# Performance work log

Hardware: AMD Instinct MI355X
Metric: run time of the kernel (lower is better)

The kernel has to match this reference:

```python
import jax, jax.numpy as jnp
import numpy as np

GH, GW = 1024, 1024  # image-like grid graph, N = GH*GW nodes


def _grid_edge_index(h, w):
    idx = np.arange(h * w, dtype=np.int32).reshape(h, w)
    r = np.concatenate([idx[:, :-1].ravel(), idx[:, 1:].ravel(), idx[:-1, :].ravel(), idx[1:, :].ravel()])
    c = np.concatenate([idx[:, 1:].ravel(), idx[:, :-1].ravel(), idx[1:, :].ravel(), idx[:-1, :].ravel()])
    return np.stack([r, c]).astype(np.int32)


def setup_inputs():
    key = jax.random.key(0)
    ks = jax.random.split(key, 10)
    n = GH * GW
    ei = jnp.asarray(_grid_edge_index(GH, GW))
    yy, xx = np.meshgrid(np.arange(GH), np.arange(GW), indexing="ij")
    pos = jnp.asarray((np.stack([xx, yy], -1).reshape(n, 2) / float(GH)).astype(np.float32))
    x = jax.random.normal(ks[0], (n, 5), jnp.float32)
    s1, s2, s3, s4 = 5 ** -0.5, 16 ** -0.5, 32 ** -0.5, 8 ** -0.5
    return {
        "x": x, "pos": pos, "edge_index": ei,
        "W1": jax.random.normal(ks[1], (5, 16), jnp.float32) * s1,
        "W1r": jax.random.normal(ks[2], (5, 16), jnp.float32) * s1,
        "b1": jnp.zeros((16,), jnp.float32),
        "W2": jax.random.normal(ks[3], (16, 32), jnp.float32) * s2,
        "W2r": jax.random.normal(ks[4], (16, 32), jnp.float32) * s2,
        "b2": jnp.zeros((32,), jnp.float32),
        "lin1_w": jax.random.normal(ks[5], (32, 8), jnp.float32) * s3,
        "lin1_b": jnp.zeros((8,), jnp.float32),
        "lin2_w": jax.random.normal(ks[6], (8, 2), jnp.float32) * s4,
        "lin2_b": jnp.zeros((2,), jnp.float32),
    }


def _spline_conv_k1(x, row, col, evalid, W, Wr, b, n):
    # SplineConv(dim=1, kernel_size=1): single basis fn == 1, edge_attr cancels.
    # out_i = mean_{(j->i)} x_j @ W + x_i @ Wr + b   (aggr='mean', target = col)
    xw = x @ W
    seg = jnp.where(evalid, col, n)  # invalid edges -> dump segment n
    msg = jnp.where(evalid[:, None], xw[row], 0.0)
    s = jax.ops.segment_sum(msg, seg, num_segments=n + 1)[:n]
    cnt = jax.ops.segment_sum(evalid.astype(x.dtype), seg, num_segments=n + 1)[:n]
    return s / jnp.maximum(cnt, 1.0)[:, None] + x @ Wr + b


def _normalized_cut(row, col, edge_attr, evalid, n):
    seg = jnp.where(evalid, row, n)
    deg = jax.ops.segment_sum(evalid.astype(edge_attr.dtype), seg, num_segments=n + 1)[:n]
    inv = jnp.where(deg > 0, 1.0 / jnp.maximum(deg, 1.0), 0.0)
    return edge_attr * (inv[row] + inv[col])


def _heavy_edge_match(row, col, w, evalid, n):
    # graclus-style heavy-edge matching, deterministic parallel mutual-max variant:
    # each node proposes its max-weight neighbor; mutual proposals merge.
    ar = jnp.arange(n, dtype=jnp.int32)
    seg = jnp.where(evalid, row, n)
    wm = jnp.where(evalid, w, -jnp.inf)
    best = jax.ops.segment_max(wm, seg, num_segments=n + 1)[:n]
    is_best = evalid & (w == best[row])
    partner = jax.ops.segment_min(jnp.where(is_best, col, n), seg, num_segments=n + 1)[:n]
    partner = jnp.where(partner >= n, ar, partner).astype(jnp.int32)
    mutual = partner[partner] == ar
    return jnp.where(mutual, jnp.minimum(ar, partner), ar)


def _forward(x, pos, edge_index, W1, W1r, b1, W2, W2r, b2, lin1_w, lin1_b, lin2_w, lin2_b):
    n = x.shape[0]
    row, col = edge_index[0], edge_index[1]
    ev0 = jnp.ones(row.shape[0], dtype=bool)
    ar = jnp.arange(n, dtype=jnp.int32)

    # GNN1: relu(SplineConv) then LeakyReLU(0.1)
    x1 = jax.nn.leaky_relu(jax.nn.relu(_spline_conv_k1(x, row, col, ev0, W1, W1r, b1, n)), 0.1)

    # normalized_cut_2d on 1-d pseudo-pos x0[:,0]; graclus; max_pool
    attr1 = jnp.abs(x[row, 0] - x[col, 0])
    c1 = _heavy_edge_match(row, col, _normalized_cut(row, col, attr1, ev0, n), ev0, n)
    valid1 = c1 == ar
    xp = jax.ops.segment_max(x1, c1, num_segments=n)  # cluster-wise max pool
    xp = jnp.where(valid1[:, None], xp, 0.0)
    cnt1 = jax.ops.segment_sum(jnp.ones((n,), x.dtype), c1, num_segments=n)
    posp = jax.ops.segment_sum(pos, c1, num_segments=n) / jnp.maximum(cnt1, 1.0)[:, None]
    row2, col2 = c1[row], c1[col]
    ev2 = row2 != col2  # drop intra-cluster (self-loop) edges

    # GNN2 (kernel_size=1 => pooled Cartesian edge_attr unused) + LeakyReLU(0.1)
    x2 = jax.nn.leaky_relu(jax.nn.relu(_spline_conv_k1(xp, row2, col2, ev2, W2, W2r, b2, n)), 0.1)

    # normalized_cut on pooled 2-d pos; graclus; max_pool_x; global_mean_pool
    d = posp[row2] - posp[col2]
    attr2 = jnp.sqrt(jnp.sum(d * d, axis=1) + 1e-12)
    c2 = _heavy_edge_match(row2, col2, _normalized_cut(row2, col2, attr2, ev2, n), ev2, n)
    seg2 = jnp.where(valid1, c2, n)
    x3 = jax.ops.segment_max(x2, seg2, num_segments=n + 1)[:n]
    cnt2 = jax.ops.segment_sum(valid1.astype(x.dtype), seg2, num_segments=n + 1)[:n]
    valid2 = cnt2 > 0
    x3 = jnp.where(valid2[:, None], x3, 0.0)
    pooled = jnp.sum(x3, axis=0) / jnp.sum(valid2.astype(x.dtype))  # single graph -> mean over clusters

    h = jax.nn.leaky_relu(pooled @ lin1_w + lin1_b, 0.1)
    return h @ lin2_w + lin2_b  # == x[0], shape [2]


def reference(x, pos, edge_index, W1, W1r, b1, W2, W2r, b2, lin1_w, lin1_b, lin2_w, lin2_b):
    return _forward(x, pos, edge_index, W1, W1r, b1, W2, W2r, b2, lin1_w, lin1_b, lin2_w, lin2_b)
```

## Files before the change

### kernel.cpp

```cpp
#include <hip/hip_runtime.h>
#include <math.h>

typedef long long i64;
typedef unsigned long long u64;

#define GWD 1024
#define GMSK 1023
#define GSH 10

__device__ __forceinline__ int xcd_band(int b, int nb) {
  return (b & 7) * (nb >> 3) + (b >> 3);
}

__device__ __forceinline__ int deg_of(int m) {
  int xx = m & GMSK, yy = m >> GSH;
  return (xx > 0) + (xx < GMSK) + (yy > 0) + (yy < GMSK);
}

__global__ __launch_bounds__(256)
void kA_match1(const float* __restrict__ x, int* __restrict__ partner1, int n) {
#pragma clang fp contract(off)
  int m = xcd_band(blockIdx.x, gridDim.x) * 256 + threadIdx.x;
  if (m >= n) return;
  int xx = m & GMSK, yy = m >> GSH;
  bool vW = xx > 0, vE = xx < GMSK, vN = yy > 0, vS = yy < GMSK;
  int cnt = (int)vW + (int)vE + (int)vN + (int)vS;
  float invi = 1.0f / (float)cnt;
  float xm0 = x[(i64)m * 5];
  float best = -INFINITY;
  int pr = n;
#define NB1(valid, J)                                                  \
  if (valid) {                                                         \
    int j = (J);                                                       \
    float a0 = x[(i64)j * 5];                                          \
    float w = fabsf(xm0 - a0) * (invi + 1.0f / (float)deg_of(j));      \
    if (w > best) { best = w; pr = j; }                                \
  }
  NB1(vN, m - GWD)
  NB1(vW, m - 1)
  NB1(vE, m + 1)
  NB1(vS, m + GWD)
#undef NB1
  partner1[m] = pr;
}

__device__ __forceinline__ void conv1_static(const float* __restrict__ x, int m,
                                             const float* w1, const float* w1r,
                                             const float* b1, float (&out)[16]) {
  int xx = m & GMSK, yy = m >> GSH;
  bool vW = xx > 0, vE = xx < GMSK, vN = yy > 0, vS = yy < GMSK;
  int cnt = (int)vW + (int)vE + (int)vN + (int)vS;
  float s0 = 0.f, s1 = 0.f, s2 = 0.f, s3 = 0.f, s4 = 0.f;
#define ACC1(valid, J)                                     \
  if (valid) {                                             \
    const float* xj = x + (i64)(J) * 5;                    \
    s0 += xj[0]; s1 += xj[1]; s2 += xj[2];                 \
    s3 += xj[3]; s4 += xj[4];                              \
  }
  ACC1(vN, m - GWD)
  ACC1(vW, m - 1)
  ACC1(vE, m + 1)
  ACC1(vS, m + GWD)
#undef ACC1
  const float* xm = x + (i64)m * 5;
  float m0 = xm[0], m1 = xm[1], m2 = xm[2], m3 = xm[3], m4 = xm[4];
  float cf = (float)cnt;
#pragma unroll
  for (int f = 0; f < 16; ++f) {
    float a  = s0 * w1[f] + s1 * w1[16 + f] + s2 * w1[32 + f] + s3 * w1[48 + f] + s4 * w1[64 + f];
    float rt = m0 * w1r[f] + m1 * w1r[16 + f] + m2 * w1r[32 + f] + m3 * w1r[48 + f] + m4 * w1r[64 + f];
    out[f] = fmaxf(a / cf + rt + b1[f], 0.0f);
  }
}

__global__ __launch_bounds__(256)
void kB_pool1(const float* __restrict__ x, const float* __restrict__ pos,
              const int* __restrict__ partner1,
              const float* __restrict__ W1, const float* __restrict__ W1r,
              const float* __restrict__ b1,
              int* __restrict__ c1, float* __restrict__ xp,
              float* __restrict__ posp, int n) {
  __shared__ float w1s[80], w1rs[80], b1s[16];
  for (int t = threadIdx.x; t < 80; t += 256) { w1s[t] = W1[t]; w1rs[t] = W1r[t]; }
  if (threadIdx.x < 16) b1s[threadIdx.x] = b1[threadIdx.x];
  __syncthreads();
  int m = xcd_band(blockIdx.x, gridDim.x) * 256 + threadIdx.x;
  if (m >= n) return;
  int p = partner1[m];
  bool mut = (partner1[p] == m);
  int head = mut ? min(m, p) : m;
  c1[m] = head;
  if (head != m) return;

  float px = pos[(i64)m * 2], py = pos[(i64)m * 2 + 1];
  if (mut) {
    px = (px + pos[(i64)p * 2]) * 0.5f;
    py = (py + pos[(i64)p * 2 + 1]) * 0.5f;
  }
  posp[(i64)m * 2] = px;
  posp[(i64)m * 2 + 1] = py;

  float v[16];
  conv1_static(x, m, w1s, w1rs, b1s, v);
  if (mut) {
    float u[16];
    conv1_static(x, p, w1s, w1rs, b1s, u);
#pragma unroll
    for (int f = 0; f < 16; ++f) v[f] = fmaxf(v[f], u[f]);
  }
#pragma unroll
  for (int f = 0; f < 16; ++f) xp[(i64)m * 16 + f] = v[f];
}

__device__ __forceinline__ int dcount(const int* __restrict__ c1, int q, int cq) {
  int xx = q & GMSK, yy = q >> GSH;
  int d = 0;
  if (yy > 0    && c1[q - GWD] != cq) ++d;
  if (xx > 0    && c1[q - 1]   != cq) ++d;
  if (xx < GMSK && c1[q + 1]   != cq) ++d;
  if (yy < GMSK && c1[q + GWD] != cq) ++d;
  return d;
}

__global__ __launch_bounds__(256)
void kC_deg2(const int* __restrict__ partner1, const int* __restrict__ c1,
             int* __restrict__ deg2, int n) {
  int m = xcd_band(blockIdx.x, gridDim.x) * 256 + threadIdx.x;
  if (m >= n) return;
  if (c1[m] != m) return;
  int p = partner1[m];
  bool mut = (partner1[p] == m);
  int d = dcount(c1, m, m);
  if (mut) d += dcount(c1, p, m);
  deg2[m] = d;
}

__global__ __launch_bounds__(256)
void kD_match2(const int* __restrict__ partner1, const int* __restrict__ c1,
               const float* __restrict__ posp, const int* __restrict__ deg2,
               int* __restrict__ partner2, int n) {
#pragma clang fp contract(off)
  int i = xcd_band(blockIdx.x, gridDim.x) * 256 + threadIdx.x;
  if (i >= n) return;
  if (c1[i] != i) return;
  int p = partner1[i];
  bool mut = (partner1[p] == i);
  float pix = posp[(i64)i * 2], piy = posp[(i64)i * 2 + 1];
  int di = deg2[i];
  float invi = (di > 0) ? 1.0f / (float)di : 0.0f;
  float best = -INFINITY;
  int bc = n;
#define NB2(valid, J)                                                   \
  if (valid) {                                                          \
    int j = (J);                                                        \
    int cu = c1[j];                                                     \
    if (cu != i) {                                                      \
      float dx = pix - posp[(i64)cu * 2];                               \
      float dy = piy - posp[(i64)cu * 2 + 1];                           \
      float attr = sqrtf((dx * dx + dy * dy) + 1e-12f);                 \
      int dc = deg2[cu];                                                \
      float invc = (dc > 0) ? 1.0f / (float)dc : 0.0f;                  \
      float w = attr * (invi + invc);                                   \
      if (w > best) { best = w; bc = cu; }                              \
      else if (w == best && cu < bc) bc = cu;                           \
    }                                                                   \
  }
  {
    int xx = i & GMSK, yy = i >> GSH;
    NB2(yy > 0, i - GWD)
    NB2(xx > 0, i - 1)
    NB2(xx < GMSK, i + 1)
    NB2(yy < GMSK, i + GWD)
  }
  if (mut) {
    int qx = p & GMSK, qy = p >> GSH;
    NB2(qy > 0, p - GWD)
    NB2(qx > 0, p - 1)
    NB2(qx < GMSK, p + 1)
    NB2(qy < GMSK, p + GWD)
  }
#undef NB2
  partner2[i] = (bc >= n) ? i : bc;
}

__device__ __forceinline__ bool l2head(const int* __restrict__ c1,
                                       const int* __restrict__ partner2, int i, int n) {
  if (i >= n || c1[i] != i) return false;
  int p2 = partner2[i];
  bool mut2 = (p2 != i) && (partner2[p2] == i);
  return !(mut2 && p2 < i);
}

__global__ __launch_bounds__(256)
void kP_count(const int* __restrict__ c1, const int* __restrict__ partner2,
              int* __restrict__ blockCounts, int n) {
  int w = xcd_band(blockIdx.x, gridDim.x);
  int i = w * 256 + threadIdx.x;
  bool a = l2head(c1, partner2, i, n);
  u64 b = __ballot(a);
  __shared__ int wc4[4];
  int lane = threadIdx.x & 63, wv = threadIdx.x >> 6;
  if (lane == 0) wc4[wv] = __popcll(b);
  __syncthreads();
  if (threadIdx.x == 0) blockCounts[w] = wc4[0] + wc4[1] + wc4[2] + wc4[3];
}

__global__ __launch_bounds__(256)
void kP_scan(const int* __restrict__ blockCounts, int* __restrict__ blockOffsets,
             int* __restrict__ countBuf, int nblk,
             const float* __restrict__ W2, const float* __restrict__ W2r,
             float* __restrict__ W2T, float* __restrict__ W2rT) {
  int t = threadIdx.x;
  for (int e = t; e < 512; e += 256) {
    int k = e >> 5, f = e & 31;
    W2T[f * 16 + k]  = W2[e];
    W2rT[f * 16 + k] = W2r[e];
  }
  __shared__ int tsum[256];
  __shared__ int toff[256];
  int per = (nblk + 255) / 256;
  int base = t * per;
  int s = 0;
  for (int k = 0; k < per; ++k) { int q = base + k; if (q < nblk) s += blockCounts[q]; }
  tsum[t] = s;
  __syncthreads();
  if (t == 0) {
    int a = 0;
    for (int k = 0; k < 256; ++k) { toff[k] = a; a += tsum[k]; }
    *countBuf = a;
  }
  __syncthreads();
  int off = toff[t];
  for (int k = 0; k < per; ++k) {
    int q = base + k;
    if (q < nblk) { blockOffsets[q] = off; off += blockCounts[q]; }
  }
}

__global__ __launch_bounds__(256)
void kP_write(const int* __restrict__ c1, const int* __restrict__ partner2,
              const int* __restrict__ blockOffsets, int* __restrict__ L, int n) {
  int w = xcd_band(blockIdx.x, gridDim.x);
  int i = w * 256 + threadIdx.x;
  bool a = l2head(c1, partner2, i, n);
  u64 b = __ballot(a);
  int lane = threadIdx.x & 63, wv = threadIdx.x >> 6;
  __shared__ int woff[4];
  if (lane == 0) woff[wv] = __popcll(b);
  __syncthreads();
  int pre = 0;
  for (int k = 0; k < wv; ++k) pre += woff[k];
  int rank = __popcll(b & ((lane == 0) ? 0ull : ((1ull << lane) - 1ull)));
  if (a) L[blockOffsets[w] + pre + rank] = i;
}

#define DECL16(P) \
  float P##0=0.f,P##1=0.f,P##2=0.f,P##3=0.f,P##4=0.f,P##5=0.f,P##6=0.f,P##7=0.f, \
        P##8=0.f,P##9=0.f,P##10=0.f,P##11=0.f,P##12=0.f,P##13=0.f,P##14=0.f,P##15=0.f

#define LOAD16(P, ptr) do { const float* _q=(ptr); \
  P##0=_q[0]; P##1=_q[1]; P##2=_q[2]; P##3=_q[3]; P##4=_q[4]; P##5=_q[5]; P##6=_q[6]; P##7=_q[7]; \
  P##8=_q[8]; P##9=_q[9]; P##10=_q[10]; P##11=_q[11]; P##12=_q[12]; P##13=_q[13]; P##14=_q[14]; P##15=_q[15]; } while(0)

#define ADD16(P, ptr) do { const float* _q=(ptr); \
  P##0+=_q[0]; P##1+=_q[1]; P##2+=_q[2]; P##3+=_q[3]; P##4+=_q[4]; P##5+=_q[5]; P##6+=_q[6]; P##7+=_q[7]; \
  P##8+=_q[8]; P##9+=_q[9]; P##10+=_q[10]; P##11+=_q[11]; P##12+=_q[12]; P##13+=_q[13]; P##14+=_q[14]; P##15+=_q[15]; } while(0)

#define MUL16(P, v) do { float _v=(v); \
  P##0*=_v; P##1*=_v; P##2*=_v; P##3*=_v; P##4*=_v; P##5*=_v; P##6*=_v; P##7*=_v; \
  P##8*=_v; P##9*=_v; P##10*=_v; P##11*=_v; P##12*=_v; P##13*=_v; P##14*=_v; P##15*=_v; } while(0)

#define GATHER_MEMBER(P, CNT, m, cid) do {                                      \
  int _m = (m); int _mx = _m & GMSK, _my = _m >> GSH;                            \
  if (_my > 0)    { int _c = c1[_m - GWD]; if (_c != (cid)) { ++CNT; ADD16(P, xp + (i64)_c * 16); } } \
  if (_mx > 0)    { int _c = c1[_m - 1];   if (_c != (cid)) { ++CNT; ADD16(P, xp + (i64)_c * 16); } } \
  if (_mx < GMSK) { int _c = c1[_m + 1];   if (_c != (cid)) { ++CNT; ADD16(P, xp + (i64)_c * 16); } } \
  if (_my < GMSK) { int _c = c1[_m + GWD]; if (_c != (cid)) { ++CNT; ADD16(P, xp + (i64)_c * 16); } } \
} while(0)

__global__ __launch_bounds__(256, 4)
void kE7_conv2_reduce(const int* __restrict__ partner1, const int* __restrict__ c1,
                      const int* __restrict__ partner2, const float* __restrict__ xp,
                      const float* __restrict__ W2T, const float* __restrict__ W2rT,
                      const float* __restrict__ b2,
                      const int* __restrict__ L, const int* __restrict__ countBuf,
                      float* __restrict__ partials) {
  int count = *countBuf;
  int nActive = (2 * count + 255) >> 8;
  int b = blockIdx.x;
  if (b >= nActive) {
    if (threadIdx.x < 33) partials[(i64)threadIdx.x * gridDim.x + b] = 0.f;
    return;
  }
  int xcd = b & 7, idx = b >> 3;
  int q = nActive >> 3, r = nActive & 7;
  int w = (xcd < r ? xcd * (q + 1) : r * (q + 1) + (xcd - r) * q) + idx;

  int gt = w * 256 + threadIdx.x;
  int pi = gt >> 1;
  int which = gt & 1;
  bool active = pi < count;
  bool doconv = false;
  DECL16(s); DECL16(hh); int cnt = 0;
  if (active) {
    int h = L[pi];
    int p2 = partner2[h];
    bool mut2 = (p2 != h) && (partner2[p2] == h);
    int myhead = which ? p2 : h;
    doconv = (which == 0) || mut2;
    if (doconv) {
      int pm = partner1[myhead];
      bool mm = (partner1[pm] == myhead);
      GATHER_MEMBER(s, cnt, myhead, myhead);
      if (mm) GATHER_MEMBER(s, cnt, pm, myhead);
      LOAD16(hh, xp + (i64)myhead * 16);
    }
  }
  float cf = (float)(cnt > 1 ? cnt : 1);
  float inv = 1.0f / cf;
  MUL16(s, inv);

  __shared__ float sm[4 * 33];
  int lane = threadIdx.x & 63, wv = threadIdx.x >> 6;

  for (int f = 0; f < 32; ++f) {
    const float4* wc = (const float4*)(W2T + (f << 4));
    float4 c0 = wc[0], c1v = wc[1], c2 = wc[2], c3 = wc[3];
    const float4* wr = (const float4*)(W2rT + (f << 4));
    float4 r0 = wr[0], r1 = wr[1], r2 = wr[2], r3 = wr[3];
    float bf = b2[f];
    float val = 0.f;
    if (doconv) {
      float a = s0 * c0.x + s1 * c0.y + s2 * c0.z + s3 * c0.w
              + s4 * c1v.x + s5 * c1v.y + s6 * c1v.z + s7 * c1v.w
              + s8 * c2.x + s9 * c2.y + s10 * c2.z + s11 * c2.w
              + s12 * c3.x + s13 * c3.y + s14 * c3.z + s15 * c3.w
              + hh0 * r0.x + hh1 * r0.y + hh2 * r0.z + hh3 * r0.w
              + hh4 * r1.x + hh5 * r1.y + hh6 * r1.z + hh7 * r1.w
              + hh8 * r2.x + hh9 * r2.y + hh10 * r2.z + hh11 * r2.w
              + hh12 * r3.x + hh13 * r3.y + hh14 * r3.z + hh15 * r3.w
              + bf;
      val = fmaxf(a, 0.0f);
    }
    float pmx = fmaxf(val, __shfl_xor(val, 1, 64));
    float contrib = pmx;
    for (int o = 32; o >= 2; o >>= 1) contrib += __shfl_down(contrib, o, 64);
    if (lane == 0) sm[wv * 33 + f] = contrib;
  }
  {
    float v = active ? 1.f : 0.f;
    for (int o = 32; o >= 2; o >>= 1) v += __shfl_down(v, o, 64);
    if (lane == 0) sm[wv * 33 + 32] = v;
  }
  __syncthreads();
  if (threadIdx.x < 33) {
    float v = sm[threadIdx.x] + sm[33 + threadIdx.x] + sm[66 + threadIdx.x] + sm[99 + threadIdx.x];
    partials[(i64)threadIdx.x * gridDim.x + b] = v;
  }
}

__global__ __launch_bounds__(256)
void kF1_rowsum(const float* __restrict__ partials, int NB, float* __restrict__ tot) {
  int r = blockIdx.x;
  const float* p = partials + (i64)r * NB;
  float a = 0.f;
  for (int k = threadIdx.x; k < NB; k += 256) a += p[k];
  __shared__ float sm[256];
  sm[threadIdx.x] = a;
  __syncthreads();
  for (int s = 128; s > 0; s >>= 1) {
    if (threadIdx.x < s) sm[threadIdx.x] += sm[threadIdx.x + s];
    __syncthreads();
  }
  if (threadIdx.x == 0) tot[r] = sm[0];
}

__global__ __launch_bounds__(64)
void kF2_mlp(const float* __restrict__ tot,
             const float* __restrict__ lin1w, const float* __restrict__ lin1b,
             const float* __restrict__ lin2w, const float* __restrict__ lin2b,
             float* __restrict__ out) {
  if (threadIdx.x != 0) return;
  float cnt = tot[32];
  float pooled[32];
#pragma unroll
  for (int f = 0; f < 32; ++f) pooled[f] = tot[f] / cnt;
  float h[8];
#pragma unroll
  for (int j = 0; j < 8; ++j) {
    float a = 0.f;
#pragma unroll
    for (int k = 0; k < 32; ++k) a += pooled[k] * lin1w[k * 8 + j];
    a += lin1b[j];
    h[j] = a >= 0.f ? a : 0.1f * a;
  }
#pragma unroll
  for (int m = 0; m < 2; ++m) {
    float a = 0.f;
#pragma unroll
    for (int j = 0; j < 8; ++j) a += h[j] * lin2w[j * 2 + m];
    out[m] = a + lin2b[m];
  }
}

extern "C" void kernel_launch(void* const* d_in, const int* in_sizes, int n_in,
                              void* d_out, int out_size, void* d_ws, size_t ws_size,
                              hipStream_t stream) {
  const float* x   = (const float*)d_in[0];
  const float* pos = (const float*)d_in[1];
  const float* W1  = (const float*)d_in[3];
  const float* W1r = (const float*)d_in[4];
  const float* b1  = (const float*)d_in[5];
  const float* W2  = (const float*)d_in[6];
  const float* W2r = (const float*)d_in[7];
  const float* b2  = (const float*)d_in[8];
  const float* l1w = (const float*)d_in[9];
  const float* l1b = (const float*)d_in[10];
  const float* l2w = (const float*)d_in[11];
  const float* l2b = (const float*)d_in[12];
  float* out = (float*)d_out;

  const int n = in_sizes[0] / 5;
  const int B = 256;
  const int gn = (n + B - 1) / B;
  const int ge = 2 * gn;

  float* base = (float*)d_ws;
  i64 off = 0;
  float* xp       = base + off; off += (i64)16 * n;
  float* posp     = base + off; off += (i64)2 * n;
  int*   partner1 = (int*)(base + off); off += n;
  int*   c1       = (int*)(base + off); off += n;
  int*   deg2     = (int*)(base + off); off += n;
  int*   partner2 = (int*)(base + off); off += n;
  int*   L        = (int*)(base + off); off += n;
  int*   blkCnt   = (int*)(base + off); off += gn;
  int*   blkOff   = (int*)(base + off); off += gn;
  int*   countBuf = (int*)(base + off); off += 1;
  off = (off + 3) & ~(i64)3;
  float* W2T      = base + off; off += 512;
  float* W2rT     = base + off; off += 512;
  float* partials = base + off; off += (i64)33 * ge;
  float* tot      = base + off; off += 33;
  (void)ws_size; (void)n_in; (void)out_size;

  kA_match1<<<gn, B, 0, stream>>>(x, partner1, n);
  kB_pool1<<<gn, B, 0, stream>>>(x, pos, partner1, W1, W1r, b1, c1, xp, posp, n);
  kC_deg2<<<gn, B, 0, stream>>>(partner1, c1, deg2, n);
  kD_match2<<<gn, B, 0, stream>>>(partner1, c1, posp, deg2, partner2, n);
  kP_count<<<gn, B, 0, stream>>>(c1, partner2, blkCnt, n);
  kP_scan<<<1, 256, 0, stream>>>(blkCnt, blkOff, countBuf, gn, W2, W2r, W2T, W2rT);
  kP_write<<<gn, B, 0, stream>>>(c1, partner2, blkOff, L, n);
  kE7_conv2_reduce<<<ge, B, 0, stream>>>(partner1, c1, partner2, xp, W2T, W2rT, b2,
                                         L, countBuf, partials);
  kF1_rowsum<<<33, 256, 0, stream>>>(partials, ge, tot);
  kF2_mlp<<<1, 64, 0, stream>>>(tot, l1w, l1b, l2w, l2b, out);
}
```

Baseline: 199.2 us.

## Precompute member/partner descriptors and pack pooled pos with inverse degree

Pool-1 now stores each node's cluster mate directly (mem1), so later kernels skip the double partner1 lookup used to test mutuality. Pooled position and the inverse degree go into one 16-byte record, so match2 fetches each neighbour with a single float4 load instead of three scattered loads plus a divide. The level-2 list now stores (head, mate) pairs, so conv2 no longer re-reads partner2. Ldesc reuses partner1's storage, and the launch_bounds occupancy hint on conv2 is dropped. The cost is more writes and wider records per node.

```diff
diff --git a/kernel.cpp b/kernel.cpp
--- a/kernel.cpp
+++ b/kernel.cpp
@@ -78,8 +78,8 @@
               const int* __restrict__ partner1,
               const float* __restrict__ W1, const float* __restrict__ W1r,
               const float* __restrict__ b1,
-              int* __restrict__ c1, float* __restrict__ xp,
-              float* __restrict__ posp, int n) {
+              int* __restrict__ c1, int* __restrict__ mem1,
+              float* __restrict__ xp, float* __restrict__ pd, int n) {
   __shared__ float w1s[80], w1rs[80], b1s[16];
   for (int t = threadIdx.x; t < 80; t += 256) { w1s[t] = W1[t]; w1rs[t] = W1r[t]; }
   if (threadIdx.x < 16) b1s[threadIdx.x] = b1[threadIdx.x];
@@ -90,6 +90,7 @@
   bool mut = (partner1[p] == m);
   int head = mut ? min(m, p) : m;
   c1[m] = head;
+  mem1[m] = mut ? p : m;
   if (head != m) return;
 
   float px = pos[(i64)m * 2], py = pos[(i64)m * 2 + 1];
@@ -97,8 +98,8 @@
     px = (px + pos[(i64)p * 2]) * 0.5f;
     py = (py + pos[(i64)p * 2 + 1]) * 0.5f;
   }
-  posp[(i64)m * 2] = px;
-  posp[(i64)m * 2 + 1] = py;
+  pd[(i64)m * 4]     = px;
+  pd[(i64)m * 4 + 1] = py;
 
   float v[16];
   conv1_static(x, m, w1s, w1rs, b1s, v);
@@ -123,31 +124,29 @@
 }
 
 __global__ __launch_bounds__(256)
-void kC_deg2(const int* __restrict__ partner1, const int* __restrict__ c1,
-             int* __restrict__ deg2, int n) {
+void kC_deg2(const int* __restrict__ mem1, const int* __restrict__ c1,
+             float* __restrict__ pd, int n) {
   int m = xcd_band(blockIdx.x, gridDim.x) * 256 + threadIdx.x;
   if (m >= n) return;
   if (c1[m] != m) return;
-  int p = partner1[m];
-  bool mut = (partner1[p] == m);
+  int p = mem1[m];
+  bool mut = (p != m);
   int d = dcount(c1, m, m);
   if (mut) d += dcount(c1, p, m);
-  deg2[m] = d;
-}
-
-__global__ __launch_bounds__(256)
-void kD_match2(const int* __restrict__ partner1, const int* __restrict__ c1,
-               const float* __restrict__ posp, const int* __restrict__ deg2,
-               int* __restrict__ partner2, int n) {
+  pd[(i64)m * 4 + 2] = (d > 0) ? 1.0f / (float)d : 0.0f;
+}
+
+__global__ __launch_bounds__(256)
+void kD_match2(const int* __restrict__ mem1, const int* __restrict__ c1,
+               const float* __restrict__ pd, int* __restrict__ partner2, int n) {
 #pragma clang fp contract(off)
   int i = xcd_band(blockIdx.x, gridDim.x) * 256 + threadIdx.x;
   if (i >= n) return;
   if (c1[i] != i) return;
-  int p = partner1[i];
-  bool mut = (partner1[p] == i);
-  float pix = posp[(i64)i * 2], piy = posp[(i64)i * 2 + 1];
-  int di = deg2[i];
-  float invi = (di > 0) ? 1.0f / (float)di : 0.0f;
+  int p = mem1[i];
+  bool mut = (p != i);
+  float4 mine = *(const float4*)(pd + (i64)i * 4);
+  float pix = mine.x, piy = mine.y, invi = mine.z;
   float best = -INFINITY;
   int bc = n;
 #define NB2(valid, J)                                                   \
@@ -155,12 +154,11 @@
     int j = (J);                                                        \
     int cu = c1[j];                                                     \
     if (cu != i) {                                                      \
-      float dx = pix - posp[(i64)cu * 2];                               \
-      float dy = piy - posp[(i64)cu * 2 + 1];                           \
+      float4 u = *(const float4*)(pd + (i64)cu * 4);                    \
+      float dx = pix - u.x;                                             \
+      float dy = piy - u.y;                                             \
       float attr = sqrtf((dx * dx + dy * dy) + 1e-12f);                 \
-      int dc = deg2[cu];                                                \
-      float invc = (dc > 0) ? 1.0f / (float)dc : 0.0f;                  \
-      float w = attr * (invi + invc);                                   \
+      float w = attr * (invi + u.z);                                    \
       if (w > best) { best = w; bc = cu; }                              \
       else if (w == best && cu < bc) bc = cu;                           \
     }                                                                   \
@@ -239,7 +237,7 @@
 
 __global__ __launch_bounds__(256)
 void kP_write(const int* __restrict__ c1, const int* __restrict__ partner2,
-              const int* __restrict__ blockOffsets, int* __restrict__ L, int n) {
+              const int* __restrict__ blockOffsets, int2* __restrict__ Ldesc, int n) {
   int w = xcd_band(blockIdx.x, gridDim.x);
   int i = w * 256 + threadIdx.x;
   bool a = l2head(c1, partner2, i, n);
@@ -251,7 +249,11 @@
   int pre = 0;
   for (int k = 0; k < wv; ++k) pre += woff[k];
   int rank = __popcll(b & ((lane == 0) ? 0ull : ((1ull << lane) - 1ull)));
-  if (a) L[blockOffsets[w] + pre + rank] = i;
+  if (a) {
+    int p2 = partner2[i];
+    bool mut2 = (p2 != i) && (partner2[p2] == i);
+    Ldesc[blockOffsets[w] + pre + rank] = make_int2(i, mut2 ? p2 : i);
+  }
 }
 
 #define DECL16(P) \
@@ -278,12 +280,12 @@
   if (_my < GMSK) { int _c = c1[_m + GWD]; if (_c != (cid)) { ++CNT; ADD16(P, xp + (i64)_c * 16); } } \
 } while(0)
 
-__global__ __launch_bounds__(256, 4)
-void kE7_conv2_reduce(const int* __restrict__ partner1, const int* __restrict__ c1,
-                      const int* __restrict__ partner2, const float* __restrict__ xp,
+__global__ __launch_bounds__(256)
+void kE9_conv2_reduce(const int* __restrict__ mem1, const int* __restrict__ c1,
+                      const float* __restrict__ xp,
                       const float* __restrict__ W2T, const float* __restrict__ W2rT,
                       const float* __restrict__ b2,
-                      const int* __restrict__ L, const int* __restrict__ countBuf,
+                      const int2* __restrict__ Ldesc, const int* __restrict__ countBuf,
                       float* __restrict__ partials) {
   int count = *countBuf;
   int nActive = (2 * count + 255) >> 8;
@@ -303,14 +305,12 @@
   bool doconv = false;
   DECL16(s); DECL16(hh); int cnt = 0;
   if (active) {
-    int h = L[pi];
-    int p2 = partner2[h];
-    bool mut2 = (p2 != h) && (partner2[p2] == h);
-    int myhead = which ? p2 : h;
-    doconv = (which == 0) || mut2;
+    int2 dsc = Ldesc[pi];
+    int myhead = which ? dsc.y : dsc.x;
+    doconv = (which == 0) || (dsc.y != dsc.x);
     if (doconv) {
-      int pm = partner1[myhead];
-      bool mm = (partner1[pm] == myhead);
+      int pm = mem1[myhead];
+      bool mm = (pm != myhead);
       GATHER_MEMBER(s, cnt, myhead, myhead);
       if (mm) GATHER_MEMBER(s, cnt, pm, myhead);
       LOAD16(hh, xp + (i64)myhead * 16);
@@ -428,12 +428,12 @@
   float* base = (float*)d_ws;
   i64 off = 0;
   float* xp       = base + off; off += (i64)16 * n;
-  float* posp     = base + off; off += (i64)2 * n;
-  int*   partner1 = (int*)(base + off); off += n;
+  float* pd       = base + off; off += (i64)4 * n;
+  int*   mem1     = (int*)(base + off); off += n;
   int*   c1       = (int*)(base + off); off += n;
-  int*   deg2     = (int*)(base + off); off += n;
   int*   partner2 = (int*)(base + off); off += n;
-  int*   L        = (int*)(base + off); off += n;
+  int*   partner1 = (int*)(base + off); off += 2 * n;
+  int2*  Ldesc    = (int2*)partner1;
   int*   blkCnt   = (int*)(base + off); off += gn;
   int*   blkOff   = (int*)(base + off); off += gn;
   int*   countBuf = (int*)(base + off); off += 1;
@@ -445,14 +445,14 @@
   (void)ws_size; (void)n_in; (void)out_size;
 
   kA_match1<<<gn, B, 0, stream>>>(x, partner1, n);
-  kB_pool1<<<gn, B, 0, stream>>>(x, pos, partner1, W1, W1r, b1, c1, xp, posp, n);
-  kC_deg2<<<gn, B, 0, stream>>>(partner1, c1, deg2, n);
-  kD_match2<<<gn, B, 0, stream>>>(partner1, c1, posp, deg2, partner2, n);
+  kB_pool1<<<gn, B, 0, stream>>>(x, pos, partner1, W1, W1r, b1, c1, mem1, xp, pd, n);
+  kC_deg2<<<gn, B, 0, stream>>>(mem1, c1, pd, n);
+  kD_match2<<<gn, B, 0, stream>>>(mem1, c1, pd, partner2, n);
   kP_count<<<gn, B, 0, stream>>>(c1, partner2, blkCnt, n);
   kP_scan<<<1, 256, 0, stream>>>(blkCnt, blkOff, countBuf, gn, W2, W2r, W2T, W2rT);
-  kP_write<<<gn, B, 0, stream>>>(c1, partner2, blkOff, L, n);
-  kE7_conv2_reduce<<<ge, B, 0, stream>>>(partner1, c1, partner2, xp, W2T, W2rT, b2,
-                                         L, countBuf, partials);
+  kP_write<<<gn, B, 0, stream>>>(c1, partner2, blkOff, Ldesc, n);
+  kE9_conv2_reduce<<<ge, B, 0, stream>>>(mem1, c1, xp, W2T, W2rT, b2,
+                                         Ldesc, countBuf, partials);
   kF1_rowsum<<<33, 256, 0, stream>>>(partials, ge, tot);
   kF2_mlp<<<1, 64, 0, stream>>>(tot, l1w, l1b, l2w, l2b, out);
 }
```

New measurement: 198.9 us. Within noise of the previous version (-0.1%).
